# Kernel tuning notes

Measured on AMD Instinct MI355X. Metric: run time of the kernel, lower is better.

The kernel has to match this reference:

```python
import jax, jax.numpy as jnp
import numpy as np

B, S, E, H = 2, 2048, 512, 8
D = E // H  # head size = 64
LN_EPS = 1e-5


def setup_inputs() -> dict:
    key = jax.random.key(0)
    ks = jax.random.split(key, 8)
    s_in = 1.0 / np.sqrt(E)
    return {
        "x": jax.random.normal(ks[0], (B, S, E), jnp.float32),
        # per-head projection weights, stored [H, E, D] so q = x @ Wq[h]
        "Wq": jax.random.normal(ks[1], (H, E, D), jnp.float32) * s_in,
        "Wk": jax.random.normal(ks[2], (H, E, D), jnp.float32) * s_in,
        "Wv": jax.random.normal(ks[3], (H, E, D), jnp.float32) * s_in,
        "Wp": jax.random.normal(ks[4], (E, E), jnp.float32) * s_in,
        "bp": jnp.zeros((E,), jnp.float32),
        "gamma": jnp.ones((E,), jnp.float32),
        "beta": jnp.zeros((E,), jnp.float32),
        # causal mask buffer: masked_fill where mask == 0
        "mask": jnp.tril(jnp.ones((S, S), jnp.int32)),
    }


def reference(x, Wq, Wk, Wv, Wp, bp, gamma, beta, mask):
    # batched per-head projections (equivalent to the H small Linears)
    q = jnp.einsum("bse,hed->bhsd", x, Wq)
    k = jnp.einsum("bse,hed->bhsd", x, Wk)
    v = jnp.einsum("bse,hed->bhsd", x, Wv)
    # NOTE: original has NO 1/sqrt(d) scaling
    att_log = jnp.einsum("bhsd,bhtd->bhst", q, k)
    att_log = jnp.where(mask == 0, -jnp.inf, att_log)
    att = jax.nn.softmax(att_log, axis=-1)
    o = jnp.einsum("bhst,bhtd->bhsd", att, v)  # [B,H,S,D]
    # torch.cat((val, values)) prepends each head -> final order head H-1 .. 0
    o = o[:, ::-1]
    vals = o.transpose(0, 2, 1, 3).reshape(B, S, E)
    out = vals @ Wp.T + bp + x
    mu = jnp.mean(out, axis=-1, keepdims=True)
    var = jnp.var(out, axis=-1, keepdims=True)
    return (out - mu) * jax.lax.rsqrt(var + LN_EPS) * gamma + beta
```

## Files before the change

### kernel.cpp

```cpp
#include <hip/hip_runtime.h>

constexpr int Bn = 2;
constexpr int Sn = 2048;
constexpr int En = 512;
constexpr int Hn = 8;
constexpr int Dn = 64;
constexpr int Mn = Bn * Sn;

typedef short bf8 __attribute__((ext_vector_type(8)));
typedef float f32x4 __attribute__((ext_vector_type(4)));

constexpr size_t XY = (size_t)Mn * En;
constexpr size_t WT = (size_t)3 * En * En;
constexpr size_t WP = (size_t)En * En;
constexpr size_t PL = (size_t)Bn * Hn * Sn * Dn;

__device__ __forceinline__ unsigned short f2bf(float f) {
    unsigned int u = __float_as_uint(f);
    unsigned int r = 0x7FFFu + ((u >> 16) & 1u);
    return (unsigned short)((u + r) >> 16);
}
__device__ __forceinline__ float bf2f(unsigned short u) {
    return __uint_as_float(((unsigned int)u) << 16);
}
__device__ __forceinline__ void split2(float f, unsigned short& hi, unsigned short& lo) {
    hi = f2bf(f);
    lo = f2bf(f - bf2f(hi));
}

__global__ __launch_bounds__(256)
void prep(const float* __restrict__ x, const float* __restrict__ Wp,
          const float* __restrict__ Wq, const float* __restrict__ Wk,
          const float* __restrict__ Wv,
          unsigned short* __restrict__ xh, unsigned short* __restrict__ xl,
          unsigned short* __restrict__ Wph, unsigned short* __restrict__ Wpl,
          unsigned short* __restrict__ Wth, unsigned short* __restrict__ Wtl)
{
    __shared__ float t[64][65];
    const int bid = blockIdx.x;
    const int tid = threadIdx.x;

    if (bid < 1152) {
        const float* src = (bid < 1024) ? x : Wp;
        unsigned short* hp = (bid < 1024) ? xh : Wph;
        unsigned short* lp = (bid < 1024) ? xl : Wpl;
        const int blk = (bid < 1024) ? bid : (bid - 1024);
        const size_t base = ((size_t)blk * 256 + tid) * 8;
        float a[8];
        *(float4*)&a[0] = *(const float4*)(src + base);
        *(float4*)&a[4] = *(const float4*)(src + base + 4);
        unsigned short h[8], l[8];
        #pragma unroll
        for (int j = 0; j < 8; ++j) split2(a[j], h[j], l[j]);
        *(bf8*)(hp + base) = *(bf8*)&h[0];
        *(bf8*)(lp + base) = *(bf8*)&l[0];
        return;
    }

    const int idx = bid - 1152;
    const int ph = idx >> 3;
    const int proj = ph >> 3, h = ph & 7;
    const int e0 = (idx & 7) * 64;
    const float* W = (proj == 0) ? Wq : (proj == 1) ? Wk : Wv;
    const float* src = W + (size_t)h * En * Dn + (size_t)e0 * Dn;

    const int er = tid >> 2, cg = (tid & 3) * 16;
    #pragma unroll
    for (int c = 0; c < 4; ++c) {
        float4 v = *(const float4*)(src + (size_t)er * Dn + cg + 4 * c);
        t[er][cg + 4 * c + 0] = v.x;
        t[er][cg + 4 * c + 1] = v.y;
        t[er][cg + 4 * c + 2] = v.z;
        t[er][cg + 4 * c + 3] = v.w;
    }
    __syncthreads();

    const int d = tid >> 2, jg = (tid & 3) * 16;
    unsigned short h16[16], l16[16];
    #pragma unroll
    for (int j = 0; j < 16; ++j) split2(t[jg + j][d], h16[j], l16[j]);
    const size_t n = (size_t)proj * 512 + h * 64 + d;
    unsigned short* dh = Wth + n * En + e0 + jg;
    unsigned short* dl = Wtl + n * En + e0 + jg;
    *(bf8*)dh       = *(bf8*)&h16[0];
    *(bf8*)(dh + 8) = *(bf8*)&h16[8];
    *(bf8*)dl       = *(bf8*)&l16[0];
    *(bf8*)(dl + 8) = *(bf8*)&l16[8];
}

__global__ __launch_bounds__(256)
void qkv_gemm(const unsigned short* __restrict__ xh,
              const unsigned short* __restrict__ xl,
              const unsigned short* __restrict__ Wth,
              const unsigned short* __restrict__ Wtl,
              unsigned short* __restrict__ qh_g,
              unsigned short* __restrict__ ql_g,
              unsigned short* __restrict__ kh_g,
              unsigned short* __restrict__ kl_g,
              unsigned short* __restrict__ vT_g)
{
    __shared__ unsigned short Ah[128][40], Al[128][40];
    __shared__ unsigned short Bh[128][40], Bl[128][40];

    const int tid = threadIdx.x;
    const int m0 = blockIdx.x * 128;
    const int n0 = blockIdx.y * 128;
    const int proj = n0 >> 9;
    const int within = n0 & 511;

    const int wave = tid >> 6, lane = tid & 63;
    const int wm = (wave >> 1) * 64, wn = (wave & 1) * 64;
    const int lm = lane & 15, quad = lane >> 4;

    const int am = tid >> 1;
    const int aks = (tid & 1) * 16;
    const unsigned short* arh = xh + (size_t)(m0 + am) * En + aks;
    const unsigned short* arl = xl + (size_t)(m0 + am) * En + aks;

    const int nn = tid & 127;
    const int bkg = (tid >> 7) * 16;
    const unsigned short* brh = Wth + (size_t)(n0 + nn) * En + bkg;
    const unsigned short* brl = Wtl + (size_t)(n0 + nn) * En + bkg;

    f32x4 acc[4][4];
    #pragma unroll
    for (int i = 0; i < 4; ++i)
        #pragma unroll
        for (int j = 0; j < 4; ++j) acc[i][j] = (f32x4){0.f, 0.f, 0.f, 0.f};

    for (int k0 = 0; k0 < En; k0 += 32) {
        *(bf8*)&Ah[am][aks]     = *(const bf8*)(arh + k0);
        *(bf8*)&Ah[am][aks + 8] = *(const bf8*)(arh + k0 + 8);
        *(bf8*)&Al[am][aks]     = *(const bf8*)(arl + k0);
        *(bf8*)&Al[am][aks + 8] = *(const bf8*)(arl + k0 + 8);
        *(bf8*)&Bh[nn][bkg]     = *(const bf8*)(brh + k0);
        *(bf8*)&Bh[nn][bkg + 8] = *(const bf8*)(brh + k0 + 8);
        *(bf8*)&Bl[nn][bkg]     = *(const bf8*)(brl + k0);
        *(bf8*)&Bl[nn][bkg + 8] = *(const bf8*)(brl + k0 + 8);
        __syncthreads();

        bf8 a_h[4], a_l[4], b_h[4], b_l[4];
        #pragma unroll
        for (int mi = 0; mi < 4; ++mi) {
            a_h[mi] = *(const bf8*)&Ah[wm + mi * 16 + lm][quad * 8];
            a_l[mi] = *(const bf8*)&Al[wm + mi * 16 + lm][quad * 8];
        }
        #pragma unroll
        for (int ni = 0; ni < 4; ++ni) {
            b_h[ni] = *(const bf8*)&Bh[wn + ni * 16 + lm][quad * 8];
            b_l[ni] = *(const bf8*)&Bl[wn + ni * 16 + lm][quad * 8];
        }
        #pragma unroll
        for (int mi = 0; mi < 4; ++mi)
            #pragma unroll
            for (int ni = 0; ni < 4; ++ni) {
                acc[mi][ni] = __builtin_amdgcn_mfma_f32_16x16x32_bf16(a_h[mi], b_h[ni], acc[mi][ni], 0, 0, 0);
                acc[mi][ni] = __builtin_amdgcn_mfma_f32_16x16x32_bf16(a_h[mi], b_l[ni], acc[mi][ni], 0, 0, 0);
                acc[mi][ni] = __builtin_amdgcn_mfma_f32_16x16x32_bf16(a_l[mi], b_h[ni], acc[mi][ni], 0, 0, 0);
            }
        __syncthreads();
    }

    if (proj < 2) {
        unsigned short* hp = (proj == 0) ? qh_g : kh_g;
        unsigned short* lp = (proj == 0) ? ql_g : kl_g;
        #pragma unroll
        for (int mi = 0; mi < 4; ++mi) {
            #pragma unroll
            for (int r = 0; r < 4; ++r) {
                const int m = m0 + wm + mi * 16 + quad * 4 + r;
                const int b = m >> 11, s = m & 2047;
                #pragma unroll
                for (int ni = 0; ni < 4; ++ni) {
                    const int nl = within + wn + ni * 16 + lm;
                    const int h = nl >> 6, d = nl & 63;
                    const size_t idx = (((size_t)(b * Hn + h) * Sn + s) * Dn) + d;
                    unsigned short hv, lv;
                    split2(acc[mi][ni][r], hv, lv);
                    hp[idx] = hv;
                    lp[idx] = lv;
                }
            }
        }
    } else {
        #pragma unroll
        for (int mi = 0; mi < 4; ++mi) {
            const int s0 = m0 + wm + mi * 16 + quad * 4;
            const int b = s0 >> 11, s = s0 & 2047;
            #pragma unroll
            for (int ni = 0; ni < 4; ++ni) {
                const int nl = within + wn + ni * 16 + lm;
                const int h = nl >> 6, d = nl & 63;
                ushort4 pk;
                pk.x = f2bf(acc[mi][ni][0]);
                pk.y = f2bf(acc[mi][ni][1]);
                pk.z = f2bf(acc[mi][ni][2]);
                pk.w = f2bf(acc[mi][ni][3]);
                *(ushort4*)(vT_g + ((size_t)(b * Hn + h) * Dn + d) * Sn + s) = pk;
            }
        }
    }
}

__global__ __launch_bounds__(256)
void attn(const unsigned short* __restrict__ qh_g,
          const unsigned short* __restrict__ ql_g,
          const unsigned short* __restrict__ kh_g,
          const unsigned short* __restrict__ kl_g,
          const unsigned short* __restrict__ vT_g,
          unsigned short* __restrict__ Op,
          float* __restrict__ ml)
{
    extern __shared__ unsigned short sm[];
    unsigned short (*khs)[72] = (unsigned short(*)[72])(sm);
    unsigned short (*kls)[72] = (unsigned short(*)[72])(sm + 4608);
    unsigned short (*vTs)[72] = (unsigned short(*)[72])(sm + 9216);
    unsigned short (*pts)[72] = (unsigned short(*)[72])(sm + 13824);
    float* alf = (float*)(sm + 18432);

    const int bidx = blockIdx.x;
    const int r_ = bidx & 255, quarter = bidx >> 8;
    const int a_ = r_ >> 4, bh = r_ & 15;
    const int qt = (quarter & 1) ? (31 - a_) : a_;
    const int hf = quarter >> 1;
    const int n0 = (qt + 2) >> 1;
    const int its = hf ? n0 : 0;
    const int ite = hf ? (qt + 1) : n0;
    const int pslot = hf * 512 + bh * 32 + qt;

    const int tid = threadIdx.x;
    const int wave = tid >> 6, lane = tid & 63;
    const int quad = lane >> 4, lq = lane & 15;

    const unsigned short* khb = kh_g + (size_t)bh * Sn * Dn;
    const unsigned short* klb = kl_g + (size_t)bh * Sn * Dn;
    const unsigned short* vTb = vT_g + (size_t)bh * Dn * Sn;

    bf8 qfh[2], qfl[2];
    {
        const size_t qoff = ((size_t)bh * Sn + (size_t)qt * 64 + wave * 16 + lq) * Dn;
        #pragma unroll
        for (int c = 0; c < 2; ++c) {
            qfh[c] = *(const bf8*)(qh_g + qoff + c * 32 + quad * 8);
            qfl[c] = *(const bf8*)(ql_g + qoff + c * 32 + quad * 8);
        }
    }

    f32x4 accO[4];
    #pragma unroll
    for (int nj = 0; nj < 4; ++nj) accO[nj] = (f32x4){0.f, 0.f, 0.f, 0.f};
    float m = -1e30f, l = 0.f;

    const int srow = tid & 63;
    const int sdg  = tid >> 6;

    bf8 pk0, pk1, pl0, pl1, pv0, pv1;
    if (its < ite) {
        const int t0 = its * 64;
        const unsigned short* kr = khb + (size_t)(t0 + srow) * Dn + sdg * 16;
        const unsigned short* lr = klb + (size_t)(t0 + srow) * Dn + sdg * 16;
        const unsigned short* vr = vTb + (size_t)srow * Sn + t0 + sdg * 16;
        pk0 = *(const bf8*)(kr);  pk1 = *(const bf8*)(kr + 8);
        pl0 = *(const bf8*)(lr);  pl1 = *(const bf8*)(lr + 8);
        pv0 = *(const bf8*)(vr);  pv1 = *(const bf8*)(vr + 8);
    }

    for (int it = its; it < ite; ++it) {
        __syncthreads();
        *(bf8*)&khs[srow][sdg * 16]     = pk0;
        *(bf8*)&khs[srow][sdg * 16 + 8] = pk1;
        *(bf8*)&kls[srow][sdg * 16]     = pl0;
        *(bf8*)&kls[srow][sdg * 16 + 8] = pl1;
        *(bf8*)&vTs[srow][sdg * 16]     = pv0;
        *(bf8*)&vTs[srow][sdg * 16 + 8] = pv1;
        __syncthreads();

        if (it + 1 < ite) {
            const int t1 = (it + 1) * 64;
            const unsigned short* kr = khb + (size_t)(t1 + srow) * Dn + sdg * 16;
            const unsigned short* lr = klb + (size_t)(t1 + srow) * Dn + sdg * 16;
            const unsigned short* vr = vTb + (size_t)srow * Sn + t1 + sdg * 16;
            pk0 = *(const bf8*)(kr);  pk1 = *(const bf8*)(kr + 8);
            pl0 = *(const bf8*)(lr);  pl1 = *(const bf8*)(lr + 8);
            pv0 = *(const bf8*)(vr);  pv1 = *(const bf8*)(vr + 8);
        }

        f32x4 accS[4];
        #pragma unroll
        for (int mi = 0; mi < 4; ++mi) accS[mi] = (f32x4){0.f, 0.f, 0.f, 0.f};
        #pragma unroll
        for (int mi = 0; mi < 4; ++mi) {
            #pragma unroll
            for (int c = 0; c < 2; ++c) {
                bf8 ah = *(const bf8*)&khs[mi * 16 + lq][c * 32 + quad * 8];
                bf8 al = *(const bf8*)&kls[mi * 16 + lq][c * 32 + quad * 8];
                accS[mi] = __builtin_amdgcn_mfma_f32_16x16x32_bf16(ah, qfh[c], accS[mi], 0, 0, 0);
                accS[mi] = __builtin_amdgcn_mfma_f32_16x16x32_bf16(ah, qfl[c], accS[mi], 0, 0, 0);
                accS[mi] = __builtin_amdgcn_mfma_f32_16x16x32_bf16(al, qfh[c], accS[mi], 0, 0, 0);
            }
        }

        if (it == qt) {
            const int qrel = wave * 16 + lq;
            #pragma unroll
            for (int mi = 0; mi < 4; ++mi)
                #pragma unroll
                for (int r = 0; r < 4; ++r)
                    if (mi * 16 + quad * 4 + r > qrel) accS[mi][r] = -INFINITY;
        }

        float mt = -INFINITY;
        #pragma unroll
        for (int mi = 0; mi < 4; ++mi)
            #pragma unroll
            for (int r = 0; r < 4; ++r) mt = fmaxf(mt, accS[mi][r]);
        mt = fmaxf(mt, __shfl_xor(mt, 16));
        mt = fmaxf(mt, __shfl_xor(mt, 32));
        const float mnew = fmaxf(m, mt);
        const float alpha = __expf(m - mnew);
        float ls = 0.f;
        #pragma unroll
        for (int mi = 0; mi < 4; ++mi)
            #pragma unroll
            for (int r = 0; r < 4; ++r) {
                const float p = __expf(accS[mi][r] - mnew);
                accS[mi][r] = p;
                ls += p;
            }
        ls += __shfl_xor(ls, 16);
        ls += __shfl_xor(ls, 32);
        l = l * alpha + ls;
        m = mnew;

        #pragma unroll
        for (int mi = 0; mi < 4; ++mi) {
            ushort4 pk;
            pk.x = f2bf(accS[mi][0]);
            pk.y = f2bf(accS[mi][1]);
            pk.z = f2bf(accS[mi][2]);
            pk.w = f2bf(accS[mi][3]);
            *(ushort4*)&pts[wave * 16 + lq][mi * 16 + quad * 4] = pk;
        }
        if (quad == 0) alf[wave * 16 + lq] = alpha;

        {
            float4 al4 = *(const float4*)&alf[wave * 16 + quad * 4];
            #pragma unroll
            for (int nj = 0; nj < 4; ++nj) {
                accO[nj][0] *= al4.x;
                accO[nj][1] *= al4.y;
                accO[nj][2] *= al4.z;
                accO[nj][3] *= al4.w;
            }
            #pragma unroll
            for (int c = 0; c < 2; ++c) {
                bf8 pf = *(const bf8*)&pts[wave * 16 + lq][c * 32 + quad * 8];
                #pragma unroll
                for (int nj = 0; nj < 4; ++nj) {
                    bf8 vf = *(const bf8*)&vTs[nj * 16 + lq][c * 32 + quad * 8];
                    accO[nj] = __builtin_amdgcn_mfma_f32_16x16x32_bf16(pf, vf, accO[nj], 0, 0, 0);
                }
            }
        }
    }

    if (quad == 0) {
        const size_t mi_ = ((size_t)pslot * 64 + wave * 16 + lq) * 2;
        ml[mi_]     = m;
        ml[mi_ + 1] = l;
    }
    #pragma unroll
    for (int r = 0; r < 4; ++r) {
        const int q = wave * 16 + quad * 4 + r;
        unsigned short* dst = Op + ((size_t)pslot * 64 + q) * 64;
        #pragma unroll
        for (int nj = 0; nj < 4; ++nj)
            dst[nj * 16 + lq] = f2bf(accO[nj][r]);
    }
}

__global__ __launch_bounds__(256)
void attn_combine(const unsigned short* __restrict__ Op,
                  const float* __restrict__ ml,
                  float* __restrict__ vals)
{
    const int bq = blockIdx.x;
    const int bh = bq >> 5, qt = bq & 31;
    const int b = bh >> 3, h = bh & 7;
    const int t = threadIdx.x;
    const int q = t >> 2, dg = (t & 3) * 16;

    const size_t p0 = (size_t)bq * 64 + q;
    const size_t p1 = (size_t)(512 + bq) * 64 + q;
    const float m0 = ml[p0 * 2], l0 = ml[p0 * 2 + 1];
    const float m1 = ml[p1 * 2], l1 = ml[p1 * 2 + 1];
    const float mn = fmaxf(m0, m1);
    const float a0 = __expf(m0 - mn), a1 = __expf(m1 - mn);
    const float inv = 1.f / (a0 * l0 + a1 * l1);

    unsigned short o0[16], o1[16];
    *(bf8*)&o0[0] = *(const bf8*)(Op + p0 * 64 + dg);
    *(bf8*)&o0[8] = *(const bf8*)(Op + p0 * 64 + dg + 8);
    *(bf8*)&o1[0] = *(const bf8*)(Op + p1 * 64 + dg);
    *(bf8*)&o1[8] = *(const bf8*)(Op + p1 * 64 + dg + 8);

    float out[16];
    #pragma unroll
    for (int j = 0; j < 16; ++j)
        out[j] = (a0 * bf2f(o0[j]) + a1 * bf2f(o1[j])) * inv;

    float* dst = vals + ((size_t)(b * Sn + qt * 64 + q)) * En
                 + (size_t)(7 - h) * 64 + dg;
    *(float4*)(dst)      = *(float4*)&out[0];
    *(float4*)(dst + 4)  = *(float4*)&out[4];
    *(float4*)(dst + 8)  = *(float4*)&out[8];
    *(float4*)(dst + 12) = *(float4*)&out[12];
}

__global__ __launch_bounds__(256)
void out_gemm(const float* __restrict__ vals,
              const unsigned short* __restrict__ Wph,
              const unsigned short* __restrict__ Wpl,
              const float* __restrict__ bp,
              const float* __restrict__ x,
              float* __restrict__ outp)
{
    __shared__ unsigned short Ah[64][40], Al[64][40];
    __shared__ unsigned short Bh[128][40], Bl[128][40];

    const int tid = threadIdx.x;
    const int m0 = blockIdx.x * 64;
    const int n0 = blockIdx.y * 128;

    const int wave = tid >> 6, lane = tid & 63;
    const int wm = (wave >> 1) * 32, wn = (wave & 1) * 64;
    const int lm = lane & 15, quad = lane >> 4;

    const int am = tid >> 2;
    const int aks = (tid & 3) * 8;
    const float* arow = vals + (size_t)(m0 + am) * En + aks;

    const int bn = tid >> 1;
    const int bks = (tid & 1) * 16;
    const unsigned short* brh = Wph + (size_t)(n0 + bn) * En + bks;
    const unsigned short* brl = Wpl + (size_t)(n0 + bn) * En + bks;

    f32x4 acc[2][4];
    #pragma unroll
    for (int i = 0; i < 2; ++i)
        #pragma unroll
        for (int j = 0; j < 4; ++j) acc[i][j] = (f32x4){0.f, 0.f, 0.f, 0.f};

    for (int k0 = 0; k0 < En; k0 += 32) {
        {
            float av[8];
            *(float4*)&av[0] = *(const float4*)(arow + k0);
            *(float4*)&av[4] = *(const float4*)(arow + k0 + 4);
            unsigned short hi[8], lo[8];
            #pragma unroll
            for (int j = 0; j < 8; ++j) split2(av[j], hi[j], lo[j]);
            *(bf8*)&Ah[am][aks] = *(bf8*)&hi[0];
            *(bf8*)&Al[am][aks] = *(bf8*)&lo[0];
        }
        *(bf8*)&Bh[bn][bks]     = *(const bf8*)(brh + k0);
        *(bf8*)&Bh[bn][bks + 8] = *(const bf8*)(brh + k0 + 8);
        *(bf8*)&Bl[bn][bks]     = *(const bf8*)(brl + k0);
        *(bf8*)&Bl[bn][bks + 8] = *(const bf8*)(brl + k0 + 8);
        __syncthreads();

        bf8 a_h[2], a_l[2], b_h[4], b_l[4];
        #pragma unroll
        for (int mi = 0; mi < 2; ++mi) {
            a_h[mi] = *(const bf8*)&Ah[wm + mi * 16 + lm][quad * 8];
            a_l[mi] = *(const bf8*)&Al[wm + mi * 16 + lm][quad * 8];
        }
        #pragma unroll
        for (int ni = 0; ni < 4; ++ni) {
            b_h[ni] = *(const bf8*)&Bh[wn + ni * 16 + lm][quad * 8];
            b_l[ni] = *(const bf8*)&Bl[wn + ni * 16 + lm][quad * 8];
        }
        #pragma unroll
        for (int mi = 0; mi < 2; ++mi)
            #pragma unroll
            for (int ni = 0; ni < 4; ++ni) {
                acc[mi][ni] = __builtin_amdgcn_mfma_f32_16x16x32_bf16(a_h[mi], b_h[ni], acc[mi][ni], 0, 0, 0);
                acc[mi][ni] = __builtin_amdgcn_mfma_f32_16x16x32_bf16(a_h[mi], b_l[ni], acc[mi][ni], 0, 0, 0);
                acc[mi][ni] = __builtin_amdgcn_mfma_f32_16x16x32_bf16(a_l[mi], b_h[ni], acc[mi][ni], 0, 0, 0);
            }
        __syncthreads();
    }

    #pragma unroll
    for (int mi = 0; mi < 2; ++mi) {
        #pragma unroll
        for (int r = 0; r < 4; ++r) {
            const int m = m0 + wm + mi * 16 + quad * 4 + r;
            #pragma unroll
            for (int ni = 0; ni < 4; ++ni) {
                const int n = n0 + wn + ni * 16 + lm;
                const size_t idx = (size_t)m * En + n;
                outp[idx] = acc[mi][ni][r] + bp[n] + x[idx];
            }
        }
    }
}

__global__ __launch_bounds__(256)
void ln_kernel(const float* __restrict__ outp,
               const float* __restrict__ gamma,
               const float* __restrict__ beta,
               float* __restrict__ y)
{
    const int row = blockIdx.x;
    const int tid = threadIdx.x;
    const float* r = outp + (size_t)row * En;

    const float a = r[tid];
    const float b = r[tid + 256];
    float sum = a + b;
    float sq = a * a + b * b;
    #pragma unroll
    for (int off = 32; off > 0; off >>= 1) {
        sum += __shfl_down(sum, off);
        sq  += __shfl_down(sq, off);
    }
    __shared__ float ls[4], lq[4];
    const int wid = tid >> 6, lane = tid & 63;
    if (lane == 0) { ls[wid] = sum; lq[wid] = sq; }
    __syncthreads();
    if (tid == 0) {
        float S = 0.f, Q = 0.f;
        #pragma unroll
        for (int w = 0; w < 4; ++w) { S += ls[w]; Q += lq[w]; }
        ls[0] = S; lq[0] = Q;
    }
    __syncthreads();
    const float mu = ls[0] * (1.f / 512.f);
    const float var = lq[0] * (1.f / 512.f) - mu * mu;
    const float rs = rsqrtf(var + 1e-5f);

    float* yr = y + (size_t)row * En;
    yr[tid]       = (a - mu) * rs * gamma[tid]       + beta[tid];
    yr[tid + 256] = (b - mu) * rs * gamma[tid + 256] + beta[tid + 256];
}

extern "C" void kernel_launch(void* const* d_in, const int* in_sizes, int n_in,
                              void* d_out, int out_size, void* d_ws, size_t ws_size,
                              hipStream_t stream)
{
    const float* x     = (const float*)d_in[0];
    const float* Wq    = (const float*)d_in[1];
    const float* Wk    = (const float*)d_in[2];
    const float* Wv    = (const float*)d_in[3];
    const float* Wp    = (const float*)d_in[4];
    const float* bp    = (const float*)d_in[5];
    const float* gamma = (const float*)d_in[6];
    const float* beta  = (const float*)d_in[7];

    float* ws   = (float*)d_ws;
    float* vals = ws;
    float* outp = ws + XY;
    unsigned short* bfb = (unsigned short*)(ws + 2 * XY);
    unsigned short* xh  = bfb;
    unsigned short* xl  = bfb + XY;
    unsigned short* Wth = bfb + 2 * XY;
    unsigned short* Wtl = Wth + WT;
    unsigned short* Wph = Wtl + WT;
    unsigned short* Wpl = Wph + WP;
    unsigned short* qh  = Wpl + WP;
    unsigned short* ql  = qh + PL;
    unsigned short* kh  = ql + PL;
    unsigned short* kl  = kh + PL;
    unsigned short* vT  = kl + PL;
    unsigned short* Op = xh;
    float* ml = outp;

    const int attn_lds = 18432 * 2 + 256;
    hipFuncSetAttribute((const void*)attn,
                        hipFuncAttributeMaxDynamicSharedMemorySize, attn_lds);

    prep<<<dim3(1344), 256, 0, stream>>>(x, Wp, Wq, Wk, Wv,
                                         xh, xl, Wph, Wpl, Wth, Wtl);
    qkv_gemm<<<dim3(Mn / 128, 12), 256, 0, stream>>>(xh, xl, Wth, Wtl,
                                                     qh, ql, kh, kl, vT);
    attn<<<dim3(1024), 256, attn_lds, stream>>>(qh, ql, kh, kl, vT, Op, ml);
    attn_combine<<<dim3(512), 256, 0, stream>>>(Op, ml, vals);
    out_gemm<<<dim3(Mn / 64, En / 128), 256, 0, stream>>>(vals, Wph, Wpl, bp, x, outp);
    ln_kernel<<<dim3(Mn), 256, 0, stream>>>(outp, gamma, beta, (float*)d_out);
}
```

Measured before the change: 184.5 us.

## Fuse attention split-combine into output GEMM, stage QKV stores via LDS, warp-per-row LayerNorm

Removes the separate attn_combine kernel. The output-projection GEMM now reads the two partial attention outputs and their max/sum statistics directly and merges them while loading its A tiles, so the fp32 vals buffer is never written or read back. The Q/K epilogue of the QKV GEMM now stages accumulators in shared memory so each thread can write 16-byte vectors of hi/lo bf16 instead of scattered 2-byte stores. LayerNorm switches to one wave per row with shuffle-only reductions and vector loads. The trade-off is redundant combine-coefficient math and duplicate partial-output reads across the four N-blocks of out_gemm, plus extra barriers in the QKV epilogue.

```diff
diff --git a/kernel.cpp b/kernel.cpp
--- a/kernel.cpp
+++ b/kernel.cpp
@@ -99,8 +99,12 @@
               unsigned short* __restrict__ kl_g,
               unsigned short* __restrict__ vT_g)
 {
-    __shared__ unsigned short Ah[128][40], Al[128][40];
-    __shared__ unsigned short Bh[128][40], Bl[128][40];
+    __shared__ __align__(16) unsigned char smraw[40960];
+    unsigned short (*Ah)[40] = (unsigned short(*)[40])(smraw);
+    unsigned short (*Al)[40] = (unsigned short(*)[40])(smraw + 10240);
+    unsigned short (*Bh)[40] = (unsigned short(*)[40])(smraw + 20480);
+    unsigned short (*Bl)[40] = (unsigned short(*)[40])(smraw + 30720);
+    float (*Cf)[132] = (float(*)[132])(smraw);
 
     const int tid = threadIdx.x;
     const int m0 = blockIdx.x * 128;
@@ -165,22 +169,42 @@
         unsigned short* hp = (proj == 0) ? qh_g : kh_g;
         unsigned short* lp = (proj == 0) ? ql_g : kl_g;
         #pragma unroll
-        for (int mi = 0; mi < 4; ++mi) {
-            #pragma unroll
-            for (int r = 0; r < 4; ++r) {
-                const int m = m0 + wm + mi * 16 + quad * 4 + r;
+        for (int p = 0; p < 2; ++p) {
+            #pragma unroll
+            for (int dmi = 0; dmi < 2; ++dmi) {
+                const int mi = 2 * p + dmi;
+                #pragma unroll
+                for (int ni = 0; ni < 4; ++ni)
+                    #pragma unroll
+                    for (int r = 0; r < 4; ++r)
+                        Cf[(wave >> 1) * 32 + dmi * 16 + quad * 4 + r]
+                          [wn + ni * 16 + lm] = acc[mi][ni][r];
+            }
+            __syncthreads();
+            {
+                const int lr = tid & 63;
+                const int cg = (tid >> 6) * 32;
+                const int m = m0 + 64 * (lr >> 5) + 32 * p + 16 * ((lr >> 4) & 1) + (lr & 15);
                 const int b = m >> 11, s = m & 2047;
+                const int ng = within + cg;
+                const int h = ng >> 6, d = ng & 63;
+                unsigned short hi[32], lo[32];
                 #pragma unroll
-                for (int ni = 0; ni < 4; ++ni) {
-                    const int nl = within + wn + ni * 16 + lm;
-                    const int h = nl >> 6, d = nl & 63;
-                    const size_t idx = (((size_t)(b * Hn + h) * Sn + s) * Dn) + d;
-                    unsigned short hv, lv;
-                    split2(acc[mi][ni][r], hv, lv);
-                    hp[idx] = hv;
-                    lp[idx] = lv;
+                for (int j4 = 0; j4 < 8; ++j4) {
+                    float4 v = *(const float4*)&Cf[lr][cg + 4 * j4];
+                    split2(v.x, hi[4 * j4 + 0], lo[4 * j4 + 0]);
+                    split2(v.y, hi[4 * j4 + 1], lo[4 * j4 + 1]);
+                    split2(v.z, hi[4 * j4 + 2], lo[4 * j4 + 2]);
+                    split2(v.w, hi[4 * j4 + 3], lo[4 * j4 + 3]);
                 }
-            }
+                const size_t base = (((size_t)(b * Hn + h) * Sn + s) * Dn) + d;
+                #pragma unroll
+                for (int c = 0; c < 4; ++c) {
+                    *(bf8*)(hp + base + 8 * c) = *(bf8*)&hi[8 * c];
+                    *(bf8*)(lp + base + 8 * c) = *(bf8*)&lo[8 * c];
+                }
+            }
+            __syncthreads();
         }
     } else {
         #pragma unroll
@@ -380,45 +404,8 @@
 }
 
 __global__ __launch_bounds__(256)
-void attn_combine(const unsigned short* __restrict__ Op,
-                  const float* __restrict__ ml,
-                  float* __restrict__ vals)
-{
-    const int bq = blockIdx.x;
-    const int bh = bq >> 5, qt = bq & 31;
-    const int b = bh >> 3, h = bh & 7;
-    const int t = threadIdx.x;
-    const int q = t >> 2, dg = (t & 3) * 16;
-
-    const size_t p0 = (size_t)bq * 64 + q;
-    const size_t p1 = (size_t)(512 + bq) * 64 + q;
-    const float m0 = ml[p0 * 2], l0 = ml[p0 * 2 + 1];
-    const float m1 = ml[p1 * 2], l1 = ml[p1 * 2 + 1];
-    const float mn = fmaxf(m0, m1);
-    const float a0 = __expf(m0 - mn), a1 = __expf(m1 - mn);
-    const float inv = 1.f / (a0 * l0 + a1 * l1);
-
-    unsigned short o0[16], o1[16];
-    *(bf8*)&o0[0] = *(const bf8*)(Op + p0 * 64 + dg);
-    *(bf8*)&o0[8] = *(const bf8*)(Op + p0 * 64 + dg + 8);
-    *(bf8*)&o1[0] = *(const bf8*)(Op + p1 * 64 + dg);
-    *(bf8*)&o1[8] = *(const bf8*)(Op + p1 * 64 + dg + 8);
-
-    float out[16];
-    #pragma unroll
-    for (int j = 0; j < 16; ++j)
-        out[j] = (a0 * bf2f(o0[j]) + a1 * bf2f(o1[j])) * inv;
-
-    float* dst = vals + ((size_t)(b * Sn + qt * 64 + q)) * En
-                 + (size_t)(7 - h) * 64 + dg;
-    *(float4*)(dst)      = *(float4*)&out[0];
-    *(float4*)(dst + 4)  = *(float4*)&out[4];
-    *(float4*)(dst + 8)  = *(float4*)&out[8];
-    *(float4*)(dst + 12) = *(float4*)&out[12];
-}
-
-__global__ __launch_bounds__(256)
-void out_gemm(const float* __restrict__ vals,
+void out_gemm(const unsigned short* __restrict__ Op,
+              const float* __restrict__ ml,
               const unsigned short* __restrict__ Wph,
               const unsigned short* __restrict__ Wpl,
               const float* __restrict__ bp,
@@ -438,7 +425,23 @@
 
     const int am = tid >> 2;
     const int aks = (tid & 3) * 8;
-    const float* arow = vals + (size_t)(m0 + am) * En + aks;
+    const int m_row = m0 + am;
+    const int b_row = m_row >> 11, s_row = m_row & 2047;
+    const int qt = s_row >> 6, qq = s_row & 63;
+
+    float c0[8], c1[8];
+    #pragma unroll
+    for (int h = 0; h < 8; ++h) {
+        const size_t base0 = (((size_t)(b_row * 8 + h) * 32 + qt) * 64 + qq) * 2;
+        const size_t base1 = base0 + (size_t)512 * 64 * 2;
+        const float m0_ = ml[base0], l0_ = ml[base0 + 1];
+        const float m1_ = ml[base1], l1_ = ml[base1 + 1];
+        const float mn = fmaxf(m0_, m1_);
+        const float a0 = __expf(m0_ - mn), a1 = __expf(m1_ - mn);
+        const float inv = 1.f / (a0 * l0_ + a1 * l1_);
+        c0[h] = a0 * inv;
+        c1[h] = a1 * inv;
+    }
 
     const int bn = tid >> 1;
     const int bks = (tid & 1) * 16;
@@ -453,12 +456,21 @@
 
     for (int k0 = 0; k0 < En; k0 += 32) {
         {
-            float av[8];
-            *(float4*)&av[0] = *(const float4*)(arow + k0);
-            *(float4*)&av[4] = *(const float4*)(arow + k0 + 4);
+            const int e0 = k0 + aks;
+            const int h = 7 - (e0 >> 6);
+            const int d = e0 & 63;
+            const size_t p0 = (((size_t)(b_row * 8 + h) * 32 + qt) * 64 + qq) * 64 + d;
+            const size_t p1 = p0 + (size_t)512 * 64 * 64;
+            bf8 o0 = *(const bf8*)(Op + p0);
+            bf8 o1 = *(const bf8*)(Op + p1);
+            const float w0 = c0[h], w1 = c1[h];
             unsigned short hi[8], lo[8];
             #pragma unroll
-            for (int j = 0; j < 8; ++j) split2(av[j], hi[j], lo[j]);
+            for (int j = 0; j < 8; ++j) {
+                const float v = w0 * bf2f((unsigned short)o0[j]) +
+                                w1 * bf2f((unsigned short)o1[j]);
+                split2(v, hi[j], lo[j]);
+            }
             *(bf8*)&Ah[am][aks] = *(bf8*)&hi[0];
             *(bf8*)&Al[am][aks] = *(bf8*)&lo[0];
         }
@@ -511,37 +523,35 @@
                const float* __restrict__ beta,
                float* __restrict__ y)
 {
-    const int row = blockIdx.x;
-    const int tid = threadIdx.x;
-    const float* r = outp + (size_t)row * En;
-
-    const float a = r[tid];
-    const float b = r[tid + 256];
-    float sum = a + b;
-    float sq = a * a + b * b;
-    #pragma unroll
-    for (int off = 32; off > 0; off >>= 1) {
-        sum += __shfl_down(sum, off);
-        sq  += __shfl_down(sq, off);
-    }
-    __shared__ float ls[4], lq[4];
-    const int wid = tid >> 6, lane = tid & 63;
-    if (lane == 0) { ls[wid] = sum; lq[wid] = sq; }
-    __syncthreads();
-    if (tid == 0) {
-        float S = 0.f, Q = 0.f;
-        #pragma unroll
-        for (int w = 0; w < 4; ++w) { S += ls[w]; Q += lq[w]; }
-        ls[0] = S; lq[0] = Q;
-    }
-    __syncthreads();
-    const float mu = ls[0] * (1.f / 512.f);
-    const float var = lq[0] * (1.f / 512.f) - mu * mu;
+    const int row = blockIdx.x * 4 + (threadIdx.x >> 6);
+    const int lane = threadIdx.x & 63;
+    const float* r = outp + (size_t)row * En + lane * 8;
+
+    float a[8];
+    *(float4*)&a[0] = *(const float4*)(r);
+    *(float4*)&a[4] = *(const float4*)(r + 4);
+
+    float sum = 0.f, sq = 0.f;
+    #pragma unroll
+    for (int j = 0; j < 8; ++j) { sum += a[j]; sq += a[j] * a[j]; }
+    #pragma unroll
+    for (int off = 1; off < 64; off <<= 1) {
+        sum += __shfl_xor(sum, off);
+        sq  += __shfl_xor(sq, off);
+    }
+    const float mu = sum * (1.f / 512.f);
+    const float var = sq * (1.f / 512.f) - mu * mu;
     const float rs = rsqrtf(var + 1e-5f);
 
-    float* yr = y + (size_t)row * En;
-    yr[tid]       = (a - mu) * rs * gamma[tid]       + beta[tid];
-    yr[tid + 256] = (b - mu) * rs * gamma[tid + 256] + beta[tid + 256];
+    const float* g = gamma + lane * 8;
+    const float* be = beta + lane * 8;
+    float o[8];
+    #pragma unroll
+    for (int j = 0; j < 8; ++j)
+        o[j] = (a[j] - mu) * rs * g[j] + be[j];
+    float* yr = y + (size_t)row * En + lane * 8;
+    *(float4*)(yr)     = *(float4*)&o[0];
+    *(float4*)(yr + 4) = *(float4*)&o[4];
 }
 
 extern "C" void kernel_launch(void* const* d_in, const int* in_sizes, int n_in,
@@ -558,7 +568,7 @@
     const float* beta  = (const float*)d_in[7];
 
     float* ws   = (float*)d_ws;
-    float* vals = ws;
+    float* ml   = ws;
     float* outp = ws + XY;
     unsigned short* bfb = (unsigned short*)(ws + 2 * XY);
     unsigned short* xh  = bfb;
@@ -573,7 +583,6 @@
     unsigned short* kl  = kh + PL;
     unsigned short* vT  = kl + PL;
     unsigned short* Op = xh;
-    float* ml = outp;
 
     const int attn_lds = 18432 * 2 + 256;
     hipFuncSetAttribute((const void*)attn,
@@ -584,7 +593,6 @@
     qkv_gemm<<<dim3(Mn / 128, 12), 256, 0, stream>>>(xh, xl, Wth, Wtl,
                                                      qh, ql, kh, kl, vT);
     attn<<<dim3(1024), 256, attn_lds, stream>>>(qh, ql, kh, kl, vT, Op, ml);
-    attn_combine<<<dim3(512), 256, 0, stream>>>(Op, ml, vals);
-    out_gemm<<<dim3(Mn / 64, En / 128), 256, 0, stream>>>(vals, Wph, Wpl, bp, x, outp);
-    ln_kernel<<<dim3(Mn), 256, 0, stream>>>(outp, gamma, beta, (float*)d_out);
-}
+    out_gemm<<<dim3(Mn / 64, En / 128), 256, 0, stream>>>(Op, ml, Wph, Wpl, bp, x, outp);
+    ln_kernel<<<dim3(Mn / 4), 256, 0, stream>>>(outp, gamma, beta, (float*)d_out);
+}
```

Result: no change. 182.9 us (-0.8%).
